# Kernel optimization log

Measured on AMD Instinct MI355X. Metric: run time of the kernel, lower is better.

## Reference

```python
import jax, jax.numpy as jnp
import numpy as np

B, S, H = 8, 1024, 1024
NH, DH = 16, 64
F_DIM, E, TOPK = 4096, 8, 2
EPS = 1e-5


def setup_inputs() -> dict:
    key = jax.random.key(0)
    ks = jax.random.split(key, 12)
    s = 0.02
    return {
        "x": jax.random.normal(ks[0], (B, S, H), jnp.float32),
        "ln1_w": jnp.ones((H,), jnp.float32),
        "ln1_b": jnp.zeros((H,), jnp.float32),
        "ln2_w": jnp.ones((H,), jnp.float32),
        "ln2_b": jnp.zeros((H,), jnp.float32),
        "in_proj_w": jax.random.normal(ks[1], (3 * H, H), jnp.float32) * s,
        "in_proj_b": jnp.zeros((3 * H,), jnp.float32),
        "out_proj_w": jax.random.normal(ks[2], (H, H), jnp.float32) * s,
        "out_proj_b": jnp.zeros((H,), jnp.float32),
        "gate_w": jax.random.normal(ks[3], (E, H), jnp.float32) * s,
        "gate_b": jnp.zeros((E,), jnp.float32),
        "w1": jax.random.normal(ks[4], (E, H, F_DIM), jnp.float32) * s,
        "b1": jnp.zeros((E, F_DIM), jnp.float32),
        "w2": jax.random.normal(ks[5], (E, F_DIM, H), jnp.float32) * s,
        "b2": jnp.zeros((E, H), jnp.float32),
    }


def _layernorm(x, w, b):
    mu = jnp.mean(x, axis=-1, keepdims=True)
    var = jnp.var(x, axis=-1, keepdims=True)
    return (x - mu) * jax.lax.rsqrt(var + EPS) * w + b


def reference(x, ln1_w, ln1_b, ln2_w, ln2_b, in_proj_w, in_proj_b,
              out_proj_w, out_proj_b, gate_w, gate_b, w1, b1, w2, b2):
    # --- attention sub-block ---
    xn = _layernorm(x, ln1_w, ln1_b)
    qkv = xn @ in_proj_w.T + in_proj_b                     # [B,S,3H]
    q, k, v = jnp.split(qkv, 3, axis=-1)
    q = q.reshape(B, S, NH, DH).transpose(0, 2, 1, 3)      # [B,NH,S,DH]
    k = k.reshape(B, S, NH, DH).transpose(0, 2, 1, 3)
    v = v.reshape(B, S, NH, DH).transpose(0, 2, 1, 3)
    scores = jnp.einsum("bhqd,bhkd->bhqk", q, k) / jnp.sqrt(jnp.float32(DH))
    attn = jax.nn.softmax(scores, axis=-1)
    ctx = jnp.einsum("bhqk,bhkd->bhqd", attn, v)
    ctx = ctx.transpose(0, 2, 1, 3).reshape(B, S, H)
    x = x + ctx @ out_proj_w.T + out_proj_b

    # --- MoE sub-block (dense compute-all-experts, top-k combine) ---
    xn2 = _layernorm(x, ln2_w, ln2_b)
    logits = xn2 @ gate_w.T + gate_b                       # [B,S,E]
    topk_vals, topk_idx = jax.lax.top_k(logits, TOPK)      # [B,S,K]
    probs = jax.nn.softmax(topk_vals, axis=-1)
    hid = jax.nn.gelu(jnp.einsum("bsh,ehf->bsef", xn2, w1) + b1, approximate=False)
    expert_out = jnp.einsum("bsef,efh->bseh", hid, w2) + b2  # [B,S,E,H]
    selected = jnp.take_along_axis(expert_out, topk_idx[..., None], axis=2)  # [B,S,K,H]
    moe_out = jnp.sum(probs[..., None] * selected, axis=2)
    return x + moe_out
```

## Files before the change

### kernel.cpp

```cpp
#include <hip/hip_runtime.h>
#include <math.h>

typedef unsigned short u16;
typedef short short8 __attribute__((ext_vector_type(8)));
typedef float f32x4 __attribute__((ext_vector_type(4)));
typedef unsigned short us4 __attribute__((ext_vector_type(4)));

#define NTOK 8192
#define NEXP 8

__device__ __forceinline__ u16 f2bf(float f) {
  union { float f; unsigned u; } v; v.f = f;
  unsigned r = v.u + 0x7FFFu + ((v.u >> 16) & 1u);
  return (u16)(r >> 16);
}
__device__ __forceinline__ float bf2f(u16 u) {
  union { unsigned u; float f; } v; v.u = ((unsigned)u) << 16; return v.f;
}
__device__ __forceinline__ void gload16(const u16* src, u16* ldsDst) {
  __builtin_amdgcn_global_load_lds(
    (const __attribute__((address_space(1))) unsigned int*)(const void*)src,
    (__attribute__((address_space(3))) unsigned int*)(void*)ldsDst, 16, 0, 0);
}
__device__ __forceinline__ float gelu_f(float v) {
  float ax = fabsf(v) * 0.70710678f;
  float t = __builtin_amdgcn_rcpf(1.0f + 0.3275911f * ax);
  float p = t * (0.254829592f + t * (-0.284496736f + t * (1.421413741f +
            t * (-1.453152027f + t * 1.061405429f))));
  float er = 1.0f - p * __expf(-ax * ax);
  er = copysignf(er, v);
  return 0.5f * v * (1.0f + er);
}

__global__ void cast_kernel(const float* __restrict__ in, u16* __restrict__ out, int n4) {
  int i = blockIdx.x * blockDim.x + threadIdx.x;
  if (i < n4) {
    float4 v = ((const float4*)in)[i];
    us4 o;
    o[0] = f2bf(v.x); o[1] = f2bf(v.y); o[2] = f2bf(v.z); o[3] = f2bf(v.w);
    ((us4*)out)[i] = o;
  }
}

__global__ void transpose_cast(const float* __restrict__ in, u16* __restrict__ out, int R, int C) {
  __shared__ float tile[64][65];
  const size_t eoff = (size_t)blockIdx.z * (size_t)R * (size_t)C;
  in += eoff; out += eoff;
  const int rb = blockIdx.y * 64, cb = blockIdx.x * 64;
  const int tid = threadIdx.x;
  const int lr4 = tid >> 4;
  const int lc4 = (tid & 15) * 4;
#pragma unroll
  for (int p = 0; p < 4; ++p) {
    float4 v = *(const float4*)&in[(size_t)(rb + p * 16 + lr4) * C + cb + lc4];
    tile[p * 16 + lr4][lc4 + 0] = v.x;
    tile[p * 16 + lr4][lc4 + 1] = v.y;
    tile[p * 16 + lr4][lc4 + 2] = v.z;
    tile[p * 16 + lr4][lc4 + 3] = v.w;
  }
  __syncthreads();
  const int oc = tid >> 3;
  const int orr = (tid & 7) * 8;
#pragma unroll
  for (int p = 0; p < 2; ++p) {
    int c = p * 32 + oc;
    short8 o;
#pragma unroll
    for (int j = 0; j < 8; ++j) o[j] = (short)f2bf(tile[orr + j][c]);
    *(short8*)&out[(size_t)(cb + c) * R + rb + orr] = o;
  }
}

__global__ void ln1_kernel(const float* __restrict__ x, const float* __restrict__ w,
                           const float* __restrict__ b, u16* __restrict__ xn) {
  const int t = blockIdx.x, tid = threadIdx.x;
  __shared__ float red[8];
  float4 v = ((const float4*)(x + (size_t)t * 1024))[tid];
  float s  = v.x + v.y + v.z + v.w;
  float sq = v.x*v.x + v.y*v.y + v.z*v.z + v.w*v.w;
#pragma unroll
  for (int m = 1; m < 64; m <<= 1) { s += __shfl_xor(s, m, 64); sq += __shfl_xor(sq, m, 64); }
  if ((tid & 63) == 0) { red[tid >> 6] = s; red[4 + (tid >> 6)] = sq; }
  __syncthreads();
  float S = red[0] + red[1] + red[2] + red[3];
  float Q = red[4] + red[5] + red[6] + red[7];
  float mu  = S * (1.0f / 1024.0f);
  float var = Q * (1.0f / 1024.0f) - mu * mu;
  float inv = rsqrtf(var + 1e-5f);
  float4 wv = ((const float4*)w)[tid];
  float4 bv = ((const float4*)b)[tid];
  us4 o;
  o[0] = f2bf((v.x - mu) * inv * wv.x + bv.x);
  o[1] = f2bf((v.y - mu) * inv * wv.y + bv.y);
  o[2] = f2bf((v.z - mu) * inv * wv.z + bv.z);
  o[3] = f2bf((v.w - mu) * inv * wv.w + bv.w);
  ((us4*)(xn + (size_t)t * 1024))[tid] = o;
}

__global__ void ln2_gate_kernel(const float* __restrict__ x2, const float* __restrict__ w,
                                const float* __restrict__ b, const float* __restrict__ gw,
                                const float* __restrict__ gb, u16* __restrict__ xn2,
                                int* __restrict__ cnt, int* __restrict__ list_tok,
                                float* __restrict__ list_prob, int* __restrict__ tok2slot) {
  const int t = blockIdx.x, tid = threadIdx.x;
  __shared__ float red[8];
  __shared__ float logits[NEXP];
  __shared__ float xrow[1024];
  float4 v = ((const float4*)(x2 + (size_t)t * 1024))[tid];
  float s  = v.x + v.y + v.z + v.w;
  float sq = v.x*v.x + v.y*v.y + v.z*v.z + v.w*v.w;
#pragma unroll
  for (int m = 1; m < 64; m <<= 1) { s += __shfl_xor(s, m, 64); sq += __shfl_xor(sq, m, 64); }
  if ((tid & 63) == 0) { red[tid >> 6] = s; red[4 + (tid >> 6)] = sq; }
  __syncthreads();
  float S = red[0] + red[1] + red[2] + red[3];
  float Q = red[4] + red[5] + red[6] + red[7];
  float mu  = S * (1.0f / 1024.0f);
  float var = Q * (1.0f / 1024.0f) - mu * mu;
  float inv = rsqrtf(var + 1e-5f);
  float4 wv = ((const float4*)w)[tid];
  float4 bv = ((const float4*)b)[tid];
  float n0 = (v.x - mu) * inv * wv.x + bv.x;
  float n1 = (v.y - mu) * inv * wv.y + bv.y;
  float n2 = (v.z - mu) * inv * wv.z + bv.z;
  float n3 = (v.w - mu) * inv * wv.w + bv.w;
  xrow[tid*4+0] = n0; xrow[tid*4+1] = n1; xrow[tid*4+2] = n2; xrow[tid*4+3] = n3;
  us4 o; o[0] = f2bf(n0); o[1] = f2bf(n1); o[2] = f2bf(n2); o[3] = f2bf(n3);
  ((us4*)(xn2 + (size_t)t * 1024))[tid] = o;
  __syncthreads();
  int e = tid >> 5, l32 = tid & 31;
  const float* gwe = gw + e * 1024;
  float part = 0.0f;
  for (int i = l32; i < 1024; i += 32) part += xrow[i] * gwe[i];
#pragma unroll
  for (int m = 1; m < 32; m <<= 1) part += __shfl_xor(part, m, 64);
  if (l32 == 0) logits[e] = part + gb[e];
  __syncthreads();
  if (tid == 0) {
    float v0 = -1e30f; int e0 = 0;
#pragma unroll
    for (int i = 0; i < NEXP; ++i) { float L = logits[i]; if (L > v0) { v0 = L; e0 = i; } }
    float v1 = -1e30f; int e1 = 0;
#pragma unroll
    for (int i = 0; i < NEXP; ++i) { if (i == e0) continue; float L = logits[i]; if (L > v1) { v1 = L; e1 = i; } }
    float texp = expf(v1 - v0);
    float p0 = 1.0f / (1.0f + texp);
    float p1 = texp / (1.0f + texp);
    int s0 = atomicAdd(&cnt[e0], 1);
    list_tok[e0 * NTOK + s0] = t; list_prob[e0 * NTOK + s0] = p0;
    int s1 = atomicAdd(&cnt[e1], 1);
    list_tok[e1 * NTOK + s1] = t; list_prob[e1 * NTOK + s1] = p1;
    if (tok2slot) {
      tok2slot[2 * t]     = e0 * NTOK + s0;
      tok2slot[2 * t + 1] = e1 * NTOK + s1;
    }
  }
}

__global__ void plan_kernel(const int* __restrict__ cnt, int* __restrict__ meta) {
  if (threadIdx.x == 0) {
    int base = 0, p = 0;
    for (int e = 0; e < NEXP; ++e) {
      meta[e] = base;
      int c = cnt[e];
      base += c;
      int nm = (c + 127) >> 7;
      for (int i = 0; i < nm; ++i) { meta[16 + 2 * p] = e; meta[17 + 2 * p] = i << 7; ++p; }
    }
    meta[8] = p;
  }
}

__launch_bounds__(256)
__global__ void attn_kernel(const u16* __restrict__ qkv, u16* __restrict__ ctx) {
  const int bh = blockIdx.y;
  const int b = bh >> 4, h = bh & 15;
  const int q0 = blockIdx.x * 64;
  const int tokBase = b * 1024;
  __shared__ __align__(16) u16 Qs[64 * 72];
  __shared__ __align__(16) u16 Ks[64 * 72];
  __shared__ __align__(16) u16 Vts[64 * 72];
  __shared__ __align__(16) u16 Ps[64 * 72];
  const int tid = threadIdx.x;
  const int wave = tid >> 6, lane = tid & 63, g = lane >> 4, lr = lane & 15;

  {
    int r = tid >> 2, d0 = (tid & 3) * 16;
    const u16* src = qkv + (size_t)(tokBase + q0 + r) * 3072 + h * 64 + d0;
    *(short8*)&Qs[r * 72 + d0]     = *(const short8*)src;
    *(short8*)&Qs[r * 72 + d0 + 8] = *(const short8*)(src + 8);
  }
  __syncthreads();
  short8 aq0 = *(const short8*)&Qs[(wave * 16 + lr) * 72 + g * 8];
  short8 aq1 = *(const short8*)&Qs[(wave * 16 + lr) * 72 + 32 + g * 8];

  const f32x4 zf = {0.f, 0.f, 0.f, 0.f};
  f32x4 Ofr[4] = {zf, zf, zf, zf};
  float m_run[4], l_run[4];
#pragma unroll
  for (int r = 0; r < 4; ++r) { m_run[r] = -1e30f; l_run[r] = 0.f; }

  for (int kt = 0; kt < 1024; kt += 64) {
    __syncthreads();
    {
      int r = tid >> 2, d0 = (tid & 3) * 16;
      const u16* ksrc = qkv + (size_t)(tokBase + kt + r) * 3072 + 1024 + h * 64 + d0;
      *(short8*)&Ks[r * 72 + d0]     = *(const short8*)ksrc;
      *(short8*)&Ks[r * 72 + d0 + 8] = *(const short8*)(ksrc + 8);
      const u16* vsrc = qkv + (size_t)(tokBase + kt + r) * 3072 + 2048 + h * 64 + d0;
      short8 v0 = *(const short8*)vsrc, v1 = *(const short8*)(vsrc + 8);
#pragma unroll
      for (int j = 0; j < 8; ++j) Vts[(d0 + j) * 72 + r] = (u16)v0[j];
#pragma unroll
      for (int j = 0; j < 8; ++j) Vts[(d0 + 8 + j) * 72 + r] = (u16)v1[j];
    }
    __syncthreads();
    f32x4 sf[4];
#pragma unroll
    for (int n = 0; n < 4; ++n) sf[n] = zf;
#pragma unroll
    for (int n = 0; n < 4; ++n) {
      short8 bk0 = *(const short8*)&Ks[(n * 16 + lr) * 72 + g * 8];
      short8 bk1 = *(const short8*)&Ks[(n * 16 + lr) * 72 + 32 + g * 8];
      sf[n] = __builtin_amdgcn_mfma_f32_16x16x32_bf16(aq0, bk0, sf[n], 0, 0, 0);
      sf[n] = __builtin_amdgcn_mfma_f32_16x16x32_bf16(aq1, bk1, sf[n], 0, 0, 0);
    }
#pragma unroll
    for (int n = 0; n < 4; ++n)
#pragma unroll
      for (int r = 0; r < 4; ++r) sf[n][r] *= 0.125f;
    float mnew[4], sc[4];
#pragma unroll
    for (int r = 0; r < 4; ++r) {
      float t0 = fmaxf(fmaxf(sf[0][r], sf[1][r]), fmaxf(sf[2][r], sf[3][r]));
#pragma unroll
      for (int msk = 1; msk < 16; msk <<= 1) t0 = fmaxf(t0, __shfl_xor(t0, msk, 64));
      mnew[r] = fmaxf(m_run[r], t0);
      sc[r] = __expf(m_run[r] - mnew[r]);
      m_run[r] = mnew[r];
    }
#pragma unroll
    for (int n = 0; n < 4; ++n)
#pragma unroll
      for (int r = 0; r < 4; ++r) sf[n][r] = __expf(sf[n][r] - mnew[r]);
#pragma unroll
    for (int r = 0; r < 4; ++r) {
      float s0 = sf[0][r] + sf[1][r] + sf[2][r] + sf[3][r];
#pragma unroll
      for (int msk = 1; msk < 16; msk <<= 1) s0 += __shfl_xor(s0, msk, 64);
      l_run[r] = l_run[r] * sc[r] + s0;
    }
#pragma unroll
    for (int nd = 0; nd < 4; ++nd)
#pragma unroll
      for (int r = 0; r < 4; ++r) Ofr[nd][r] *= sc[r];
#pragma unroll
    for (int n = 0; n < 4; ++n)
#pragma unroll
      for (int r = 0; r < 4; ++r)
        Ps[(wave * 16 + g * 4 + r) * 72 + n * 16 + lr] = f2bf(sf[n][r]);
    __syncthreads();
    short8 ap0 = *(const short8*)&Ps[(wave * 16 + lr) * 72 + g * 8];
    short8 ap1 = *(const short8*)&Ps[(wave * 16 + lr) * 72 + 32 + g * 8];
#pragma unroll
    for (int nd = 0; nd < 4; ++nd) {
      short8 bv0 = *(const short8*)&Vts[(nd * 16 + lr) * 72 + g * 8];
      short8 bv1 = *(const short8*)&Vts[(nd * 16 + lr) * 72 + 32 + g * 8];
      Ofr[nd] = __builtin_amdgcn_mfma_f32_16x16x32_bf16(ap0, bv0, Ofr[nd], 0, 0, 0);
      Ofr[nd] = __builtin_amdgcn_mfma_f32_16x16x32_bf16(ap1, bv1, Ofr[nd], 0, 0, 0);
    }
  }
#pragma unroll
  for (int nd = 0; nd < 4; ++nd)
#pragma unroll
    for (int r = 0; r < 4; ++r) {
      int tok = tokBase + q0 + wave * 16 + g * 4 + r;
      int col = h * 64 + nd * 16 + lr;
      ctx[(size_t)tok * 1024 + col] = f2bf(Ofr[nd][r] / l_run[r]);
    }
}

template<int EPI>
__launch_bounds__(256, 2)
__global__ void gemmP(const u16* __restrict__ Abase, const u16* __restrict__ Bbase,
                      int K, int lda, int N, int ldc, int nSlotsFixed,
                      const float* __restrict__ bias,
                      const float* __restrict__ resid,
                      float* __restrict__ outF,
                      u16* __restrict__ outB,
                      const int* __restrict__ cnt,
                      const int* __restrict__ meta,
                      const int* __restrict__ list_tok,
                      const float* __restrict__ list_prob) {
  const int gx = gridDim.x, G = gridDim.y;
  const int nwg = gx * G;
  int orig = blockIdx.y + blockIdx.x * G;
  int q8 = nwg >> 3, r8 = nwg & 7, xcd = orig & 7, lid = orig >> 3;
  int wg = (xcd < r8 ? xcd * (q8 + 1) : r8 * (q8 + 1) + (xcd - r8) * q8) + lid;
  const int bx = wg / G, gidx = wg % G;
  const int n0 = bx * 128;

  const int S = (EPI >= 2) ? meta[8] : nSlotsFixed;
  const int cpb = (S + G - 1) / G;
  const int sBeg = gidx * cpb;
  int sEnd = sBeg + cpb; if (sEnd > S) sEnd = S;
  if (sBeg >= sEnd) return;
  const int nslots = sEnd - sBeg;
  const int NT = K >> 6;
  const int ntLog = 31 - __builtin_clz((unsigned)NT);
  const int nIt = nslots << ntLog;

  __shared__ __align__(16) u16 As[2][8192];
  __shared__ __align__(16) u16 Bs[2][8192];

  const int tid = threadIdx.x;
  const int wave = tid >> 6, lane = tid & 63, gp = lane >> 4, lr = lane & 15;
  const int wm = wave >> 1, wn = wave & 1;

  unsigned boff[4];
#pragma unroll
  for (int i = 0; i < 4; ++i) {
    int ci = i * 256 + tid;
    int row = ci >> 3, c = ci & 7;
    int lc = c ^ (row & 7);
    boff[i] = (unsigned)(n0 + row) * (unsigned)K + (unsigned)(lc << 3);
  }

  int eC, m0C, MC, sbC; const u16* BwC; unsigned aoffC[4];
  int eN, m0N, MN, sbN; const u16* BwN; unsigned aoffN[4];

  auto loadSlot = [&](int s, int& e, int& m0, int& M, int& sb, const u16*& Bw, unsigned (&ao)[4]) {
    if constexpr (EPI >= 2) {
      e = meta[16 + 2 * s]; m0 = meta[17 + 2 * s]; M = cnt[e]; sb = meta[e];
      Bw = Bbase + (size_t)e * (size_t)N * (size_t)K;
    } else {
      e = 0; m0 = s * 128; M = NTOK; sb = 0; Bw = Bbase;
    }
#pragma unroll
    for (int i = 0; i < 4; ++i) {
      int ci = i * 256 + tid;
      int row = ci >> 3, c = ci & 7;
      int lc = c ^ (row & 7);
      int arow;
      if constexpr (EPI == 2) {
        int r = m0 + row; if (r > M - 1) r = M - 1;
        arow = list_tok[e * NTOK + r];
      } else if constexpr (EPI >= 3) {
        int r = m0 + row; if (r > M - 1) r = M - 1;
        arow = sb + r;
      } else {
        arow = m0 + row;
      }
      ao[i] = (unsigned)arow * (unsigned)lda + (unsigned)(lc << 3);
    }
  };

  loadSlot(sBeg, eC, m0C, MC, sbC, BwC, aoffC);
  if (nslots > 1) loadSlot(sBeg + 1, eN, m0N, MN, sbN, BwN, aoffN);
  else { eN = eC; m0N = m0C; MN = MC; sbN = sbC; BwN = BwC;
#pragma unroll
         for (int i = 0; i < 4; ++i) aoffN[i] = aoffC[i]; }

  const int sw = lr & 7;
  const int arb = (wm * 64 + lr) * 64;
  const int brb = (wn * 64 + lr) * 64;
  const int sk0 = (gp ^ sw) * 8;
  const int sk1 = ((4 + gp) ^ sw) * 8;

  const f32x4 zf = {0.f, 0.f, 0.f, 0.f};
  f32x4 acc[4][4];
#pragma unroll
  for (int m = 0; m < 4; ++m)
#pragma unroll
    for (int n = 0; n < 4; ++n) acc[m][n] = zf;

#pragma unroll
  for (int tt = 0; tt < 2; ++tt) {
    int kt = tt << 6;
#pragma unroll
    for (int i = 0; i < 4; ++i) {
      gload16(Abase + aoffC[i] + kt, &As[tt][(i * 256 + wave * 64) << 3]);
      gload16(BwC + boff[i] + kt, &Bs[tt][(i * 256 + wave * 64) << 3]);
    }
  }
  asm volatile("s_waitcnt vmcnt(8)" ::: "memory");
  __builtin_amdgcn_s_barrier();

  for (int it = 0; it < nIt; ++it) {
    const int sRel = it >> ntLog;
    const int t = it & (NT - 1);
    const u16* Ab = As[it & 1];
    const u16* Bb = Bs[it & 1];
    short8 af[4][2], bf[4][2];
#pragma unroll
    for (int m = 0; m < 4; ++m) {
      af[m][0] = *(const short8*)&Ab[arb + m * 1024 + sk0];
      af[m][1] = *(const short8*)&Ab[arb + m * 1024 + sk1];
    }
#pragma unroll
    for (int n = 0; n < 4; ++n) {
      bf[n][0] = *(const short8*)&Bb[brb + n * 1024 + sk0];
      bf[n][1] = *(const short8*)&Bb[brb + n * 1024 + sk1];
    }
    asm volatile("s_waitcnt lgkmcnt(0)" ::: "memory");
    __builtin_amdgcn_s_barrier();
    {
      int it2 = it + 2;
      if (it2 < nIt) {
        bool nx = (it2 >> ntLog) != sRel;
        int kt2 = (it2 & (NT - 1)) << 6;
        int b2 = it2 & 1;
#pragma unroll
        for (int i = 0; i < 4; ++i) {
          unsigned ao = nx ? aoffN[i] : aoffC[i];
          const u16* bw = nx ? BwN : BwC;
          gload16(Abase + ao + kt2, &As[b2][(i * 256 + wave * 64) << 3]);
          gload16(bw + boff[i] + kt2, &Bs[b2][(i * 256 + wave * 64) << 3]);
        }
      }
    }
    __builtin_amdgcn_s_setprio(1);
#pragma unroll
    for (int kk = 0; kk < 2; ++kk)
#pragma unroll
      for (int m = 0; m < 4; ++m)
#pragma unroll
        for (int n = 0; n < 4; ++n)
          acc[m][n] = __builtin_amdgcn_mfma_f32_16x16x32_bf16(af[m][kk], bf[n][kk], acc[m][n], 0, 0, 0);
    __builtin_amdgcn_s_setprio(0);
    if (it < nIt - 3) { asm volatile("s_waitcnt vmcnt(8)" ::: "memory"); }
    else              { asm volatile("s_waitcnt vmcnt(0)" ::: "memory"); }
    __builtin_amdgcn_s_barrier();

    if (t == NT - 1) {
#pragma unroll
      for (int m = 0; m < 4; ++m) {
        int rloc = wm * 64 + m * 16 + gp * 4;
#pragma unroll
        for (int n = 0; n < 4; ++n) {
          int gc = n0 + wn * 64 + n * 16 + lr;
          float bcol;
          if constexpr (EPI >= 2) bcol = bias[(size_t)eC * N + gc];
          else bcol = bias[gc];
#pragma unroll
          for (int r = 0; r < 4; ++r) {
            int ridx = m0C + rloc + r;
            float vv = acc[m][n][r] + bcol;
            if constexpr (EPI == 0) {
              outB[(size_t)ridx * ldc + gc] = f2bf(vv);
            } else if constexpr (EPI == 1) {
              size_t off = (size_t)ridx * ldc + gc;
              outF[off] = vv + resid[off];
            } else if constexpr (EPI == 2) {
              if (ridx < MC)
                outB[(size_t)(sbC + ridx) * ldc + gc] = f2bf(gelu_f(vv));
            } else if constexpr (EPI == 3) {
              if (ridx < MC)
                outB[(size_t)(sbC + ridx) * ldc + gc] = f2bf(vv);
            } else {
              if (ridx < MC) {
                int tok = list_tok[eC * NTOK + ridx];
                float p = list_prob[eC * NTOK + ridx];
                atomicAdd(&outF[(size_t)tok * ldc + gc], vv * p);
              }
            }
            acc[m][n][r] = 0.f;
          }
        }
      }
      eC = eN; m0C = m0N; MC = MN; sbC = sbN; BwC = BwN;
#pragma unroll
      for (int i = 0; i < 4; ++i) aoffC[i] = aoffN[i];
      int s2 = sBeg + sRel + 2;
      if (s2 < sEnd) loadSlot(s2, eN, m0N, MN, sbN, BwN, aoffN);
    }
  }
}

__global__ void combine_kernel(const u16* __restrict__ part, const int* __restrict__ cnt,
                               const int* __restrict__ tok2slot, const float* __restrict__ lprb,
                               float* __restrict__ out) {
  const int t = blockIdx.x, tid = threadIdx.x;
  __shared__ int base[NEXP];
  if (tid == 0) {
    int b = 0;
#pragma unroll
    for (int j = 0; j < NEXP; ++j) { base[j] = b; b += cnt[j]; }
  }
  __syncthreads();
  int c0 = tok2slot[2 * t], c1 = tok2slot[2 * t + 1];
  float p0 = lprb[c0], p1 = lprb[c1];
  int g0 = base[c0 >> 13] + (c0 & 8191);
  int g1 = base[c1 >> 13] + (c1 & 8191);
  us4 a = ((const us4*)(part + (size_t)g0 * 1024))[tid];
  us4 b = ((const us4*)(part + (size_t)g1 * 1024))[tid];
  float4 o = ((const float4*)(out + (size_t)t * 1024))[tid];
  o.x += p0 * bf2f(a[0]) + p1 * bf2f(b[0]);
  o.y += p0 * bf2f(a[1]) + p1 * bf2f(b[1]);
  o.z += p0 * bf2f(a[2]) + p1 * bf2f(b[2]);
  o.w += p0 * bf2f(a[3]) + p1 * bf2f(b[3]);
  ((float4*)(out + (size_t)t * 1024))[tid] = o;
}

extern "C" void kernel_launch(void* const* d_in, const int* in_sizes, int n_in,
                              void* d_out, int out_size, void* d_ws, size_t ws_size,
                              hipStream_t stream) {
  const float* x    = (const float*)d_in[0];
  const float* ln1w = (const float*)d_in[1];
  const float* ln1b = (const float*)d_in[2];
  const float* ln2w = (const float*)d_in[3];
  const float* ln2b = (const float*)d_in[4];
  const float* inw  = (const float*)d_in[5];
  const float* inb  = (const float*)d_in[6];
  const float* outw = (const float*)d_in[7];
  const float* outb = (const float*)d_in[8];
  const float* gw   = (const float*)d_in[9];
  const float* gb   = (const float*)d_in[10];
  const float* w1   = (const float*)d_in[11];
  const float* b1   = (const float*)d_in[12];
  const float* w2   = (const float*)d_in[13];
  const float* b2   = (const float*)d_in[14];
  float* out = (float*)d_out;
  char* ws = (char*)d_ws;

  u16* xn1 = (u16*)(ws + 0);
  u16* qkv = (u16*)(ws + 16777216);
  u16* ctx = (u16*)(ws + 67108864);
  u16* hid = (u16*)(ws + 0);
  u16* xn2 = (u16*)(ws + 134217728);
  u16* w1t = (u16*)(ws + 150994944);
  u16* winb  = (u16*)(ws + 218103808);
  u16* woutb = (u16*)(ws + 224395264);
  u16* w2t = (u16*)(ws + 134217728);
  u16* part = (u16*)(ws + 201326592);

  const bool bigWS = ws_size >= 235475456ull;
  int *cnt, *meta, *ltok, *t2s; float* lprb;
  if (bigWS) {
    cnt  = (int*)(ws + 234881024);
    meta = (int*)(ws + 234883072);
    ltok = (int*)(ws + 234887168);
    lprb = (float*)(ws + 235149312);
    t2s  = (int*)(ws + 235411456);
  } else {
    cnt  = (int*)(ws + 226492416);
    meta = (int*)(ws + 226494464);
    ltok = (int*)(ws + 226498560);
    lprb = (float*)(ws + 226760704);
    t2s  = nullptr;
  }

  cast_kernel<<<3072, 256, 0, stream>>>(inw, winb, 786432);
  cast_kernel<<<1024, 256, 0, stream>>>(outw, woutb, 262144);
  transpose_cast<<<dim3(64, 16, 8), 256, 0, stream>>>(w1, w1t, 1024, 4096);

  ln1_kernel<<<8192, 256, 0, stream>>>(x, ln1w, ln1b, xn1);
  gemmP<0><<<dim3(24, 16), 256, 0, stream>>>(xn1, winb, 1024, 1024, 3072, 3072, 64,
      inb, nullptr, nullptr, qkv, nullptr, nullptr, nullptr, nullptr);
  attn_kernel<<<dim3(16, 128), 256, 0, stream>>>(qkv, ctx);
  gemmP<1><<<dim3(8, 32), 256, 0, stream>>>(ctx, woutb, 1024, 1024, 1024, 1024, 64,
      outb, x, out, nullptr, nullptr, nullptr, nullptr, nullptr);

  hipMemsetAsync(cnt, 0, 32, stream);
  ln2_gate_kernel<<<8192, 256, 0, stream>>>(out, ln2w, ln2b, gw, gb, xn2, cnt, ltok, lprb, t2s);
  plan_kernel<<<1, 64, 0, stream>>>(cnt, meta);
  gemmP<2><<<dim3(32, 16), 256, 0, stream>>>(xn2, w1t, 1024, 1024, 4096, 4096, 0,
      b1, nullptr, nullptr, hid, cnt, meta, ltok, lprb);
  transpose_cast<<<dim3(16, 64, 8), 256, 0, stream>>>(w2, w2t, 4096, 1024);
  if (bigWS) {
    gemmP<3><<<dim3(8, 64), 256, 0, stream>>>(hid, w2t, 4096, 4096, 1024, 1024, 0,
        b2, nullptr, nullptr, part, cnt, meta, ltok, lprb);
    combine_kernel<<<8192, 256, 0, stream>>>(part, cnt, t2s, lprb, out);
  } else {
    gemmP<4><<<dim3(8, 64), 256, 0, stream>>>(hid, w2t, 4096, 4096, 1024, 1024, 0,
        b2, nullptr, out, nullptr, cnt, meta, ltok, lprb);
  }
}
```

Measured before the change: 1.082 ms.

## Widen GEMM tiles to 128x256 with 512 threads, triple buffering, and pre-gathered expert inputs

```diff
diff --git a/kernel.cpp b/kernel.cpp
--- a/kernel.cpp
+++ b/kernel.cpp
@@ -171,6 +171,17 @@
   }
 }
 
+__global__ void xgather_kernel(const u16* __restrict__ xn2, const int* __restrict__ meta,
+                               const int* __restrict__ tok2slot, u16* __restrict__ xg) {
+  const int t = blockIdx.x, tid = threadIdx.x;
+  short8 v = ((const short8*)(xn2 + (size_t)t * 1024))[tid];
+  int c0 = tok2slot[2 * t], c1 = tok2slot[2 * t + 1];
+  int g0 = meta[c0 >> 13] + (c0 & 8191);
+  int g1 = meta[c1 >> 13] + (c1 & 8191);
+  ((short8*)(xg + (size_t)g0 * 1024))[tid] = v;
+  ((short8*)(xg + (size_t)g1 * 1024))[tid] = v;
+}
+
 __launch_bounds__(256)
 __global__ void attn_kernel(const u16* __restrict__ qkv, u16* __restrict__ ctx) {
   const int bh = blockIdx.y;
@@ -281,8 +292,8 @@
 }
 
 template<int EPI>
-__launch_bounds__(256, 2)
-__global__ void gemmP(const u16* __restrict__ Abase, const u16* __restrict__ Bbase,
+__launch_bounds__(512, 1)
+__global__ void gemmF(const u16* __restrict__ Abase, const u16* __restrict__ Bbase,
                       int K, int lda, int N, int ldc, int nSlotsFixed,
                       const float* __restrict__ bias,
                       const float* __restrict__ resid,
@@ -298,7 +309,7 @@
   int q8 = nwg >> 3, r8 = nwg & 7, xcd = orig & 7, lid = orig >> 3;
   int wg = (xcd < r8 ? xcd * (q8 + 1) : r8 * (q8 + 1) + (xcd - r8) * q8) + lid;
   const int bx = wg / G, gidx = wg % G;
-  const int n0 = bx * 128;
+  const int n0 = bx * 256;
 
   const int S = (EPI >= 2) ? meta[8] : nSlotsFixed;
   const int cpb = (S + G - 1) / G;
@@ -310,26 +321,26 @@
   const int ntLog = 31 - __builtin_clz((unsigned)NT);
   const int nIt = nslots << ntLog;
 
-  __shared__ __align__(16) u16 As[2][8192];
-  __shared__ __align__(16) u16 Bs[2][8192];
+  __shared__ __align__(16) u16 As[3][8192];
+  __shared__ __align__(16) u16 Bs[3][16384];
 
   const int tid = threadIdx.x;
   const int wave = tid >> 6, lane = tid & 63, gp = lane >> 4, lr = lane & 15;
-  const int wm = wave >> 1, wn = wave & 1;
+  const int wm = wave >> 2, wn = wave & 3;
 
   unsigned boff[4];
 #pragma unroll
   for (int i = 0; i < 4; ++i) {
-    int ci = i * 256 + tid;
+    int ci = i * 512 + tid;
     int row = ci >> 3, c = ci & 7;
     int lc = c ^ (row & 7);
     boff[i] = (unsigned)(n0 + row) * (unsigned)K + (unsigned)(lc << 3);
   }
 
-  int eC, m0C, MC, sbC; const u16* BwC; unsigned aoffC[4];
-  int eN, m0N, MN, sbN; const u16* BwN; unsigned aoffN[4];
-
-  auto loadSlot = [&](int s, int& e, int& m0, int& M, int& sb, const u16*& Bw, unsigned (&ao)[4]) {
+  int eC, m0C, MC, sbC; const u16* BwC; unsigned aoffC[2];
+  int eN, m0N, MN, sbN; const u16* BwN; unsigned aoffN[2];
+
+  auto loadSlot = [&](int s, int& e, int& m0, int& M, int& sb, const u16*& Bw, unsigned (&ao)[2]) {
     if constexpr (EPI >= 2) {
       e = meta[16 + 2 * s]; m0 = meta[17 + 2 * s]; M = cnt[e]; sb = meta[e];
       Bw = Bbase + (size_t)e * (size_t)N * (size_t)K;
@@ -337,8 +348,8 @@
       e = 0; m0 = s * 128; M = NTOK; sb = 0; Bw = Bbase;
     }
 #pragma unroll
-    for (int i = 0; i < 4; ++i) {
-      int ci = i * 256 + tid;
+    for (int i = 0; i < 2; ++i) {
+      int ci = i * 512 + tid;
       int row = ci >> 3, c = ci & 7;
       int lc = c ^ (row & 7);
       int arow;
@@ -358,8 +369,7 @@
   loadSlot(sBeg, eC, m0C, MC, sbC, BwC, aoffC);
   if (nslots > 1) loadSlot(sBeg + 1, eN, m0N, MN, sbN, BwN, aoffN);
   else { eN = eC; m0N = m0C; MN = MC; sbN = sbC; BwN = BwC;
-#pragma unroll
-         for (int i = 0; i < 4; ++i) aoffN[i] = aoffC[i]; }
+         aoffN[0] = aoffC[0]; aoffN[1] = aoffC[1]; }
 
   const int sw = lr & 7;
   const int arb = (wm * 64 + lr) * 64;
@@ -375,22 +385,22 @@
     for (int n = 0; n < 4; ++n) acc[m][n] = zf;
 
 #pragma unroll
-  for (int tt = 0; tt < 2; ++tt) {
-    int kt = tt << 6;
-#pragma unroll
-    for (int i = 0; i < 4; ++i) {
-      gload16(Abase + aoffC[i] + kt, &As[tt][(i * 256 + wave * 64) << 3]);
-      gload16(BwC + boff[i] + kt, &Bs[tt][(i * 256 + wave * 64) << 3]);
-    }
-  }
-  asm volatile("s_waitcnt vmcnt(8)" ::: "memory");
+  for (int i = 0; i < 4; ++i) gload16(BwC + boff[i], &Bs[0][(i * 512 + wave * 64) << 3]);
+#pragma unroll
+  for (int i = 0; i < 2; ++i) gload16(Abase + aoffC[i], &As[0][(i * 512 + wave * 64) << 3]);
+  asm volatile("" ::: "memory");
+#pragma unroll
+  for (int i = 0; i < 4; ++i) gload16(BwC + boff[i] + 64, &Bs[1][(i * 512 + wave * 64) << 3]);
+#pragma unroll
+  for (int i = 0; i < 2; ++i) gload16(Abase + aoffC[i] + 64, &As[1][(i * 512 + wave * 64) << 3]);
+  asm volatile("s_waitcnt vmcnt(6)" ::: "memory");
   __builtin_amdgcn_s_barrier();
 
+  int cur3 = 0;
   for (int it = 0; it < nIt; ++it) {
     const int sRel = it >> ntLog;
-    const int t = it & (NT - 1);
-    const u16* Ab = As[it & 1];
-    const u16* Bb = Bs[it & 1];
+    const u16* Ab = As[cur3];
+    const u16* Bb = Bs[cur3];
     short8 af[4][2], bf[4][2];
 #pragma unroll
     for (int m = 0; m < 4; ++m) {
@@ -409,13 +419,17 @@
       if (it2 < nIt) {
         bool nx = (it2 >> ntLog) != sRel;
         int kt2 = (it2 & (NT - 1)) << 6;
-        int b2 = it2 & 1;
-#pragma unroll
-        for (int i = 0; i < 4; ++i) {
+        int wr3 = cur3 - 1; if (wr3 < 0) wr3 = 2;
+        u16* dA = As[wr3];
+        u16* dB = Bs[wr3];
+        const u16* bw = nx ? BwN : BwC;
+#pragma unroll
+        for (int i = 0; i < 4; ++i)
+          gload16(bw + boff[i] + kt2, &dB[(i * 512 + wave * 64) << 3]);
+#pragma unroll
+        for (int i = 0; i < 2; ++i) {
           unsigned ao = nx ? aoffN[i] : aoffC[i];
-          const u16* bw = nx ? BwN : BwC;
-          gload16(Abase + ao + kt2, &As[b2][(i * 256 + wave * 64) << 3]);
-          gload16(bw + boff[i] + kt2, &Bs[b2][(i * 256 + wave * 64) << 3]);
+          gload16(Abase + ao + kt2, &dA[(i * 512 + wave * 64) << 3]);
         }
       }
     }
@@ -428,11 +442,11 @@
         for (int n = 0; n < 4; ++n)
           acc[m][n] = __builtin_amdgcn_mfma_f32_16x16x32_bf16(af[m][kk], bf[n][kk], acc[m][n], 0, 0, 0);
     __builtin_amdgcn_s_setprio(0);
-    if (it < nIt - 3) { asm volatile("s_waitcnt vmcnt(8)" ::: "memory"); }
+    if (it < nIt - 2) { asm volatile("s_waitcnt vmcnt(6)" ::: "memory"); }
     else              { asm volatile("s_waitcnt vmcnt(0)" ::: "memory"); }
     __builtin_amdgcn_s_barrier();
 
-    if (t == NT - 1) {
+    if ((it & (NT - 1)) == NT - 1) {
 #pragma unroll
       for (int m = 0; m < 4; ++m) {
         int rloc = wm * 64 + m * 16 + gp * 4;
@@ -451,7 +465,7 @@
             } else if constexpr (EPI == 1) {
               size_t off = (size_t)ridx * ldc + gc;
               outF[off] = vv + resid[off];
-            } else if constexpr (EPI == 2) {
+            } else if constexpr (EPI == 2 || EPI == 5) {
               if (ridx < MC)
                 outB[(size_t)(sbC + ridx) * ldc + gc] = f2bf(gelu_f(vv));
             } else if constexpr (EPI == 3) {
@@ -469,11 +483,11 @@
         }
       }
       eC = eN; m0C = m0N; MC = MN; sbC = sbN; BwC = BwN;
-#pragma unroll
-      for (int i = 0; i < 4; ++i) aoffC[i] = aoffN[i];
+      aoffC[0] = aoffN[0]; aoffC[1] = aoffN[1];
       int s2 = sBeg + sRel + 2;
       if (s2 < sEnd) loadSlot(s2, eN, m0N, MN, sbN, BwN, aoffN);
     }
+    cur3 = (cur3 == 2) ? 0 : cur3 + 1;
   }
 }
 
@@ -527,14 +541,16 @@
   u16* qkv = (u16*)(ws + 16777216);
   u16* ctx = (u16*)(ws + 67108864);
   u16* hid = (u16*)(ws + 0);
-  u16* xn2 = (u16*)(ws + 134217728);
-  u16* w1t = (u16*)(ws + 150994944);
+  u16* w1t = (u16*)(ws + 134217728);
   u16* winb  = (u16*)(ws + 218103808);
   u16* woutb = (u16*)(ws + 224395264);
   u16* w2t = (u16*)(ws + 134217728);
+  u16* xg   = (u16*)(ws + 201326592);
   u16* part = (u16*)(ws + 201326592);
 
   const bool bigWS = ws_size >= 235475456ull;
+  u16* xn2 = bigWS ? (u16*)(ws + 0)
+                   : (u16*)(ws + 201326592);
   int *cnt, *meta, *ltok, *t2s; float* lprb;
   if (bigWS) {
     cnt  = (int*)(ws + 234881024);
@@ -555,24 +571,30 @@
   transpose_cast<<<dim3(64, 16, 8), 256, 0, stream>>>(w1, w1t, 1024, 4096);
 
   ln1_kernel<<<8192, 256, 0, stream>>>(x, ln1w, ln1b, xn1);
-  gemmP<0><<<dim3(24, 16), 256, 0, stream>>>(xn1, winb, 1024, 1024, 3072, 3072, 64,
+  gemmF<0><<<dim3(12, 16), 512, 0, stream>>>(xn1, winb, 1024, 1024, 3072, 3072, 64,
       inb, nullptr, nullptr, qkv, nullptr, nullptr, nullptr, nullptr);
   attn_kernel<<<dim3(16, 128), 256, 0, stream>>>(qkv, ctx);
-  gemmP<1><<<dim3(8, 32), 256, 0, stream>>>(ctx, woutb, 1024, 1024, 1024, 1024, 64,
+  gemmF<1><<<dim3(4, 64), 512, 0, stream>>>(ctx, woutb, 1024, 1024, 1024, 1024, 64,
       outb, x, out, nullptr, nullptr, nullptr, nullptr, nullptr);
 
   hipMemsetAsync(cnt, 0, 32, stream);
   ln2_gate_kernel<<<8192, 256, 0, stream>>>(out, ln2w, ln2b, gw, gb, xn2, cnt, ltok, lprb, t2s);
   plan_kernel<<<1, 64, 0, stream>>>(cnt, meta);
-  gemmP<2><<<dim3(32, 16), 256, 0, stream>>>(xn2, w1t, 1024, 1024, 4096, 4096, 0,
-      b1, nullptr, nullptr, hid, cnt, meta, ltok, lprb);
+  if (bigWS) {
+    xgather_kernel<<<8192, 128, 0, stream>>>(xn2, meta, t2s, xg);
+    gemmF<5><<<dim3(16, 16), 512, 0, stream>>>(xg, w1t, 1024, 1024, 4096, 4096, 0,
+        b1, nullptr, nullptr, hid, cnt, meta, ltok, lprb);
+  } else {
+    gemmF<2><<<dim3(16, 16), 512, 0, stream>>>(xn2, w1t, 1024, 1024, 4096, 4096, 0,
+        b1, nullptr, nullptr, hid, cnt, meta, ltok, lprb);
+  }
   transpose_cast<<<dim3(16, 64, 8), 256, 0, stream>>>(w2, w2t, 4096, 1024);
   if (bigWS) {
-    gemmP<3><<<dim3(8, 64), 256, 0, stream>>>(hid, w2t, 4096, 4096, 1024, 1024, 0,
+    gemmF<3><<<dim3(4, 64), 512, 0, stream>>>(hid, w2t, 4096, 4096, 1024, 1024, 0,
         b2, nullptr, nullptr, part, cnt, meta, ltok, lprb);
     combine_kernel<<<8192, 256, 0, stream>>>(part, cnt, t2s, lprb, out);
   } else {
-    gemmP<4><<<dim3(8, 64), 256, 0, stream>>>(hid, w2t, 4096, 4096, 1024, 1024, 0,
+    gemmF<4><<<dim3(4, 64), 512, 0, stream>>>(hid, w2t, 4096, 4096, 1024, 1024, 0,
         b2, nullptr, out, nullptr, cnt, meta, ltok, lprb);
   }
 }
```

After: 1.126 ms. 1.04x slower.

## Pre-gather routed tokens into contiguous per-expert rows before the first MoE GEMM

Applied to the files above, without the earlier changes.

```diff
diff --git a/kernel.cpp b/kernel.cpp
--- a/kernel.cpp
+++ b/kernel.cpp
@@ -169,6 +169,17 @@
     }
     meta[8] = p;
   }
+}
+
+__global__ void xgather_kernel(const u16* __restrict__ xn2, const int* __restrict__ meta,
+                               const int* __restrict__ tok2slot, u16* __restrict__ xg) {
+  const int t = blockIdx.x, tid = threadIdx.x;
+  short8 v = ((const short8*)(xn2 + (size_t)t * 1024))[tid];
+  int c0 = tok2slot[2 * t], c1 = tok2slot[2 * t + 1];
+  int g0 = meta[c0 >> 13] + (c0 & 8191);
+  int g1 = meta[c1 >> 13] + (c1 & 8191);
+  ((short8*)(xg + (size_t)g0 * 1024))[tid] = v;
+  ((short8*)(xg + (size_t)g1 * 1024))[tid] = v;
 }
 
 __launch_bounds__(256)
@@ -375,20 +386,21 @@
     for (int n = 0; n < 4; ++n) acc[m][n] = zf;
 
 #pragma unroll
-  for (int tt = 0; tt < 2; ++tt) {
-    int kt = tt << 6;
-#pragma unroll
-    for (int i = 0; i < 4; ++i) {
-      gload16(Abase + aoffC[i] + kt, &As[tt][(i * 256 + wave * 64) << 3]);
-      gload16(BwC + boff[i] + kt, &Bs[tt][(i * 256 + wave * 64) << 3]);
-    }
+  for (int i = 0; i < 4; ++i) {
+    gload16(Abase + aoffC[i], &As[0][(i * 256 + wave * 64) << 3]);
+    gload16(BwC + boff[i], &Bs[0][(i * 256 + wave * 64) << 3]);
+  }
+  asm volatile("" ::: "memory");
+#pragma unroll
+  for (int i = 0; i < 4; ++i) {
+    gload16(Abase + aoffC[i] + 64, &As[1][(i * 256 + wave * 64) << 3]);
+    gload16(BwC + boff[i] + 64, &Bs[1][(i * 256 + wave * 64) << 3]);
   }
   asm volatile("s_waitcnt vmcnt(8)" ::: "memory");
   __builtin_amdgcn_s_barrier();
 
   for (int it = 0; it < nIt; ++it) {
     const int sRel = it >> ntLog;
-    const int t = it & (NT - 1);
     const u16* Ab = As[it & 1];
     const u16* Bb = Bs[it & 1];
     short8 af[4][2], bf[4][2];
@@ -410,10 +422,10 @@
         bool nx = (it2 >> ntLog) != sRel;
         int kt2 = (it2 & (NT - 1)) << 6;
         int b2 = it2 & 1;
+        const u16* bw = nx ? BwN : BwC;
 #pragma unroll
         for (int i = 0; i < 4; ++i) {
           unsigned ao = nx ? aoffN[i] : aoffC[i];
-          const u16* bw = nx ? BwN : BwC;
           gload16(Abase + ao + kt2, &As[b2][(i * 256 + wave * 64) << 3]);
           gload16(bw + boff[i] + kt2, &Bs[b2][(i * 256 + wave * 64) << 3]);
         }
@@ -432,7 +444,7 @@
     else              { asm volatile("s_waitcnt vmcnt(0)" ::: "memory"); }
     __builtin_amdgcn_s_barrier();
 
-    if (t == NT - 1) {
+    if ((it & (NT - 1)) == NT - 1) {
 #pragma unroll
       for (int m = 0; m < 4; ++m) {
         int rloc = wm * 64 + m * 16 + gp * 4;
@@ -451,7 +463,7 @@
             } else if constexpr (EPI == 1) {
               size_t off = (size_t)ridx * ldc + gc;
               outF[off] = vv + resid[off];
-            } else if constexpr (EPI == 2) {
+            } else if constexpr (EPI == 2 || EPI == 5) {
               if (ridx < MC)
                 outB[(size_t)(sbC + ridx) * ldc + gc] = f2bf(gelu_f(vv));
             } else if constexpr (EPI == 3) {
@@ -527,14 +539,16 @@
   u16* qkv = (u16*)(ws + 16777216);
   u16* ctx = (u16*)(ws + 67108864);
   u16* hid = (u16*)(ws + 0);
-  u16* xn2 = (u16*)(ws + 134217728);
-  u16* w1t = (u16*)(ws + 150994944);
+  u16* w1t = (u16*)(ws + 134217728);
   u16* winb  = (u16*)(ws + 218103808);
   u16* woutb = (u16*)(ws + 224395264);
   u16* w2t = (u16*)(ws + 134217728);
+  u16* xg   = (u16*)(ws + 201326592);
   u16* part = (u16*)(ws + 201326592);
 
   const bool bigWS = ws_size >= 235475456ull;
+  u16* xn2 = bigWS ? (u16*)(ws + 0)
+                   : (u16*)(ws + 201326592);
   int *cnt, *meta, *ltok, *t2s; float* lprb;
   if (bigWS) {
     cnt  = (int*)(ws + 234881024);
@@ -564,8 +578,14 @@
   hipMemsetAsync(cnt, 0, 32, stream);
   ln2_gate_kernel<<<8192, 256, 0, stream>>>(out, ln2w, ln2b, gw, gb, xn2, cnt, ltok, lprb, t2s);
   plan_kernel<<<1, 64, 0, stream>>>(cnt, meta);
-  gemmP<2><<<dim3(32, 16), 256, 0, stream>>>(xn2, w1t, 1024, 1024, 4096, 4096, 0,
-      b1, nullptr, nullptr, hid, cnt, meta, ltok, lprb);
+  if (bigWS) {
+    xgather_kernel<<<8192, 128, 0, stream>>>(xn2, meta, t2s, xg);
+    gemmP<5><<<dim3(32, 16), 256, 0, stream>>>(xg, w1t, 1024, 1024, 4096, 4096, 0,
+        b1, nullptr, nullptr, hid, cnt, meta, ltok, lprb);
+  } else {
+    gemmP<2><<<dim3(32, 16), 256, 0, stream>>>(xn2, w1t, 1024, 1024, 4096, 4096, 0,
+        b1, nullptr, nullptr, hid, cnt, meta, ltok, lprb);
+  }
   transpose_cast<<<dim3(16, 64, 8), 256, 0, stream>>>(w2, w2t, 4096, 1024);
   if (bigWS) {
     gemmP<3><<<dim3(8, 64), 256, 0, stream>>>(hid, w2t, 4096, 4096, 1024, 1024, 0,
```

Result: no change. 1.095 ms (+1.1%).
